# Optimization experiments

Hardware: AMD Instinct MI355X
Metric: run time of the kernel (lower is better)

Reference implementation:

```python
import jax, jax.numpy as jnp
import numpy as np

DIM = 768
D_STATE = 16
D_INNER = 2 * DIM  # expand=2


def setup_inputs() -> dict:
    key = jax.random.key(0)
    k_x, k_in, k_conv, k_out = jax.random.split(key, 4)
    B, L = 1, 4096
    x = jax.random.normal(k_x, (B, L, DIM), dtype=jnp.float32)
    # torch Linear weight layout: [out_features, in_features]
    W_in = jax.random.normal(k_in, (3 * D_INNER + 2 * D_STATE, DIM), dtype=jnp.float32) * 0.02
    # depthwise conv1d kernel: [out_ch=d_inner, in_ch/groups=1, k=3]
    W_conv = jax.random.normal(k_conv, (D_INNER, 1, 3), dtype=jnp.float32) * 0.1
    W_out = jax.random.normal(k_out, (DIM, D_INNER), dtype=jnp.float32) * 0.02
    A_log = jnp.log(jnp.tile(jnp.arange(1, D_STATE + 1, dtype=jnp.float32), (D_INNER, 1)))
    D = jnp.ones((D_INNER,), dtype=jnp.float32)
    return {"x": x, "W_in": W_in, "W_conv": W_conv, "W_out": W_out, "A_log": A_log, "D": D}


def reference(x, W_in, W_conv, W_out, A_log, D):
    d_inner = W_conv.shape[0]
    d_state = A_log.shape[1]
    Bsz = x.shape[0]

    xz = x @ W_in.T  # [B, L, 3*d_inner + 2*d_state]
    x_inner, z, B_ssm, C_ssm, delta = jnp.split(
        xz, [d_inner, 2 * d_inner, 2 * d_inner + d_state, 2 * d_inner + 2 * d_state], axis=-1
    )

    # depthwise conv over sequence: [B, d_inner, L]
    xc = jax.lax.conv_general_dilated(
        x_inner.transpose(0, 2, 1), W_conv,
        window_strides=(1,), padding=[(1, 1)], feature_group_count=d_inner,
    ).transpose(0, 2, 1)  # back to [B, L, d_inner]
    xc = jax.nn.silu(xc)

    A = -jnp.exp(A_log)  # [d_inner, d_state]
    delta = jax.nn.softplus(delta)  # [B, L, d_inner]
    dA = jnp.exp(jnp.einsum('bld,dn->bldn', delta, A))           # [B, L, d_inner, d_state]
    dBx = jnp.einsum('bld,bln,bld->bldn', delta, B_ssm, xc)      # delta_B * x fused

    def step(h, inp):
        da_t, dbx_t, c_t = inp  # [B,d,n], [B,d,n], [B,n]
        h = da_t * h + dbx_t
        y_t = jnp.einsum('bdn,bn->bd', h, c_t)
        return h, y_t

    h0 = jnp.zeros((Bsz, d_inner, d_state), dtype=x.dtype)
    _, ys = jax.lax.scan(
        step, h0,
        (dA.transpose(1, 0, 2, 3), dBx.transpose(1, 0, 2, 3), C_ssm.transpose(1, 0, 2)),
    )  # ys: [L, B, d_inner]

    y = ys.transpose(1, 0, 2) + xc * D  # skip connection
    y = y * jax.nn.silu(z)
    return y @ W_out.T  # [B, L, dim]
```

## Files before the change

### kernel.cpp

```cpp
#include <hip/hip_runtime.h>
#include <hip/hip_bf16.h>
#include <math.h>

#define LSEQ   4096
#define DIM    768
#define DINNER 1536
#define DSTATE 16
#define NCOLS  4640
#define NCH    128
#define CLEN   32
#define NPAD   4736
#define DXW    1568

typedef _Float16 f16;
typedef __attribute__((ext_vector_type(8))) _Float16 f16x8;
typedef __attribute__((ext_vector_type(4))) float f32x4;

__device__ __forceinline__ void gld_lds16(void* lds_dst, const void* gsrc) {
    __builtin_amdgcn_global_load_lds(
        (__attribute__((address_space(1))) void*)(gsrc),
        (__attribute__((address_space(3))) void*)(lds_dst), 16, 0, 0);
}

#define G1K    768
#define G1_NT  12
#define G1_BM  256
#define G1_BN  128
#define G1_RT  384
#define G1_LDSE (G1_RT * 64)

__global__ __launch_bounds__(512) void gemm1_pipe(const f16* __restrict__ A,
                                                  const f16* __restrict__ B,
                                                  float* __restrict__ C,
                                                  f16* __restrict__ Xb,
                                                  f16* __restrict__ Zb) {
    __shared__ __align__(16) f16 S[3 * G1_LDSE];

    const int P   = gridDim.x >> 3;
    const int idx = (blockIdx.x & 7) * P + (blockIdx.x >> 3);
    const int m0  = (idx & 15) * G1_BM;
    const int n0  = (idx >> 4) * G1_BN;

    const int tid  = threadIdx.x;
    const int w    = tid >> 6;
    const int lane = tid & 63;
    const int wr   = w >> 1;
    const int wc   = w & 1;
    const int m    = lane & 15;
    const int q    = lane >> 4;
    const int rl8  = lane >> 3;
    const int bsel = lane & 7;

    const f16* gb[6];
#pragma unroll
    for (int s = 0; s < 6; ++s) {
        const int rl  = (w + 8 * s) * 8 + rl8;
        const int blk = bsel ^ (rl & 7);
        gb[s] = (rl < G1_BM) ? A + (size_t)(m0 + rl) * G1K + blk * 8
                             : B + (size_t)(n0 + rl - G1_BM) * G1K + blk * 8;
    }

    f32x4 acc[4][4];
#pragma unroll
    for (int i = 0; i < 4; i++)
#pragma unroll
        for (int j = 0; j < 4; j++) acc[i][j] = (f32x4){0.f, 0.f, 0.f, 0.f};

    auto stg = [&](int kt) {
        f16* dst = S + (kt % 3) * G1_LDSE;
#pragma unroll
        for (int s = 0; s < 6; ++s)
            gld_lds16(dst + (w + 8 * s) * 512, gb[s] + kt * 64);
    };

    stg(0);
    stg(1);

#pragma unroll
    for (int kt = 0; kt < G1_NT; ++kt) {
        if (kt < G1_NT - 1) asm volatile("s_waitcnt vmcnt(6)" ::: "memory");
        else                asm volatile("s_waitcnt vmcnt(0)" ::: "memory");
        __builtin_amdgcn_s_barrier();
        if (kt + 2 < G1_NT) stg(kt + 2);

        const f16* As = S + (kt % 3) * G1_LDSE;
        const f16* Bs = As + G1_BM * 64;
        __builtin_amdgcn_s_setprio(1);
#pragma unroll
        for (int kk = 0; kk < 2; kk++) {
            const int fo = (((q + 4 * kk) ^ (m & 7)) << 3);
            f16x8 af[4], bh[4];
#pragma unroll
            for (int i = 0; i < 4; i++)
                af[i] = *(const f16x8*)&As[(wr * 64 + i * 16 + m) * 64 + fo];
#pragma unroll
            for (int j = 0; j < 4; j++)
                bh[j] = *(const f16x8*)&Bs[(wc * 64 + j * 16 + m) * 64 + fo];
#pragma unroll
            for (int i = 0; i < 4; i++)
#pragma unroll
                for (int j = 0; j < 4; j++)
                    acc[i][j] = __builtin_amdgcn_mfma_f32_16x16x32_f16(
                        af[i], bh[j], acc[i][j], 0, 0, 0);
        }
        __builtin_amdgcn_s_setprio(0);
    }

    if (n0 < DINNER) {
#pragma unroll
        for (int i = 0; i < 4; i++)
#pragma unroll
            for (int j = 0; j < 4; j++) {
                const int col  = n0 + wc * 64 + j * 16 + m;
                const int rowb = m0 + wr * 64 + i * 16 + q * 4;
#pragma unroll
                for (int r = 0; r < 4; r++)
                    Xb[(size_t)(rowb + r) * DINNER + col] = (f16)acc[i][j][r];
            }
        return;
    }
    if (n0 < 2 * DINNER) {
#pragma unroll
        for (int i = 0; i < 4; i++)
#pragma unroll
            for (int j = 0; j < 4; j++) {
                const int col  = n0 - DINNER + wc * 64 + j * 16 + m;
                const int rowb = m0 + wr * 64 + i * 16 + q * 4;
#pragma unroll
                for (int r = 0; r < 4; r++)
                    Zb[(size_t)(rowb + r) * DINNER + col] = (f16)acc[i][j][r];
            }
        return;
    }
#pragma unroll
    for (int i = 0; i < 4; i++)
#pragma unroll
        for (int j = 0; j < 4; j++) {
            const int col = n0 - 2 * DINNER + wc * 64 + j * 16 + m;
            if (col >= DXW) continue;
            const int rowb = m0 + wr * 64 + i * 16 + q * 4;
#pragma unroll
            for (int r = 0; r < 4; r++)
                C[(size_t)(rowb + r) * DXW + col] = acc[i][j][r];
        }
}

template<int BM, int BN, int WM, int WN, int NTB, bool COLM, bool ZMODE>
__global__ __launch_bounds__(256) void gemm_f16(const f16* __restrict__ A,
                                                const f16* __restrict__ B,
                                                float* __restrict__ C,
                                                f16* __restrict__ Xb,
                                                f16* __restrict__ Zb,
                                                int M, int N, int K, int ldc) {
    constexpr int MI  = WM / 16;
    constexpr int NI  = WN / 16;
    constexpr int NWN = BN / WN;
    constexpr int RT  = BM + BN;
    constexpr int NS  = RT / 8;

    __shared__ __align__(16) f16 S[RT * 64];
    f16* As = S;
    f16* Bs = S + BM * 64;

    const int P   = gridDim.x >> 3;
    const int idx = (blockIdx.x & 7) * P + (blockIdx.x >> 3);
    const int m0  = (COLM ? (idx % NTB) : (idx / NTB)) * BM;
    const int n0  = (COLM ? (idx / NTB) : (idx % NTB)) * BN;

    const int tid  = threadIdx.x;
    const int w    = tid >> 6;
    const int lane = tid & 63;
    const int wr   = w / NWN;
    const int wc   = w % NWN;
    const int m    = lane & 15;
    const int q    = lane >> 4;
    const int rl8  = lane >> 3;
    const int bsel = lane & 7;

    f32x4 acc[MI][NI];
#pragma unroll
    for (int i = 0; i < MI; i++)
#pragma unroll
        for (int j = 0; j < NI; j++) acc[i][j] = (f32x4){0.f, 0.f, 0.f, 0.f};

    for (int k0 = 0; k0 < K; k0 += 64) {
#pragma unroll
        for (int t = w; t < NS; t += 4) {
            const int rl  = t * 8 + rl8;
            const int blk = bsel ^ (rl & 7);
            const f16* g = (rl < BM)
                ? A + (size_t)(m0 + rl) * K + k0 + blk * 8
                : B + (size_t)(n0 + rl - BM) * K + k0 + blk * 8;
            gld_lds16(S + t * 8 * 64, g);
        }
        __syncthreads();

#pragma unroll
        for (int kk = 0; kk < 2; kk++) {
            const int fo = (((q + 4 * kk) ^ (m & 7)) << 3);
            f16x8 af[MI], bh[NI];
#pragma unroll
            for (int i = 0; i < MI; i++)
                af[i] = *(const f16x8*)&As[(wr * WM + i * 16 + m) * 64 + fo];
#pragma unroll
            for (int j = 0; j < NI; j++)
                bh[j] = *(const f16x8*)&Bs[(wc * WN + j * 16 + m) * 64 + fo];
#pragma unroll
            for (int i = 0; i < MI; i++)
#pragma unroll
                for (int j = 0; j < NI; j++)
                    acc[i][j] = __builtin_amdgcn_mfma_f32_16x16x32_f16(
                        af[i], bh[j], acc[i][j], 0, 0, 0);
        }
        __syncthreads();
    }

    if (ZMODE && n0 < DINNER) {
#pragma unroll
        for (int i = 0; i < MI; i++)
#pragma unroll
            for (int j = 0; j < NI; j++) {
                const int col  = n0 + wc * WN + j * 16 + m;
                const int rowb = m0 + wr * WM + i * 16 + q * 4;
#pragma unroll
                for (int r = 0; r < 4; r++)
                    Xb[(size_t)(rowb + r) * DINNER + col] = (f16)acc[i][j][r];
            }
        return;
    }
    if (ZMODE && n0 < 2 * DINNER) {
#pragma unroll
        for (int i = 0; i < MI; i++)
#pragma unroll
            for (int j = 0; j < NI; j++) {
                const int col  = n0 - DINNER + wc * WN + j * 16 + m;
                const int rowb = m0 + wr * WM + i * 16 + q * 4;
#pragma unroll
                for (int r = 0; r < 4; r++)
                    Zb[(size_t)(rowb + r) * DINNER + col] = (f16)acc[i][j][r];
            }
        return;
    }
#pragma unroll
    for (int i = 0; i < MI; i++)
#pragma unroll
        for (int j = 0; j < NI; j++) {
            const int col  = (ZMODE ? n0 - 2 * DINNER : n0) + wc * WN + j * 16 + m;
            const int lim  = ZMODE ? DXW : N;
            if (col >= lim) continue;
            const int rowb = m0 + wr * WM + i * 16 + q * 4;
#pragma unroll
            for (int r = 0; r < 4; r++)
                C[(size_t)(rowb + r) * ldc + col] = acc[i][j][r];
        }
}

#define E0 (LSEQ * DIM)
#define E1 (E0 + NPAD * DIM)
#define E2 (E1 + DIM * DINNER)

__global__ __launch_bounds__(256) void cvt_all(const float* __restrict__ x,
                                               const float* __restrict__ Wi,
                                               const float* __restrict__ Wo,
                                               f16* __restrict__ Ax,
                                               f16* __restrict__ Bw,
                                               f16* __restrict__ Bo) {
    int i = (blockIdx.x * 256 + threadIdx.x) * 4;
    if (i < E0) {
        float4 v = *(const float4*)(x + i);
        Ax[i] = (f16)v.x; Ax[i+1] = (f16)v.y; Ax[i+2] = (f16)v.z; Ax[i+3] = (f16)v.w;
    } else if (i < E1) {
        int e = i - E0;
        int n = e / DIM;
        if (n < NCOLS) {
            float4 v = *(const float4*)(Wi + e);
            Bw[e] = (f16)v.x; Bw[e+1] = (f16)v.y; Bw[e+2] = (f16)v.z; Bw[e+3] = (f16)v.w;
        } else {
            Bw[e] = (f16)0.f; Bw[e+1] = (f16)0.f; Bw[e+2] = (f16)0.f; Bw[e+3] = (f16)0.f;
        }
    } else if (i < E2) {
        int e = i - E1;
        float4 v = *(const float4*)(Wo + e);
        Bo[e] = (f16)v.x; Bo[e+1] = (f16)v.y; Bo[e+2] = (f16)v.z; Bo[e+3] = (f16)v.w;
    }
}

__global__ __launch_bounds__(256) void scan1_kernel(const float* __restrict__ Dxz,
                                                    const f16* __restrict__ Xb,
                                                    const float* __restrict__ Wc,
                                                    const float* __restrict__ A_log,
                                                    float* __restrict__ aprod,
                                                    float* __restrict__ hend) {
    __shared__ float Bs[CLEN * DSTATE];
    const int d  = blockIdx.x * 256 + threadIdx.x;
    const int c  = blockIdx.y;
    const int l0 = c * CLEN;
    for (int i = threadIdx.x; i < CLEN * DSTATE; i += 256)
        Bs[i] = Dxz[(size_t)(l0 + (i >> 4)) * DXW + (i & 15)];
    float Areg[DSTATE];
#pragma unroll
    for (int n = 0; n < DSTATE; n++) Areg[n] = -__expf(A_log[d * DSTATE + n]);
    const float w0 = Wc[d * 3 + 0], w1 = Wc[d * 3 + 1], w2 = Wc[d * 3 + 2];
    float xm = (l0 > 0) ? (float)Xb[(size_t)(l0 - 1) * DINNER + d] : 0.f;
    float x0 = (float)Xb[(size_t)l0 * DINNER + d];
    float ld_xp   = (float)Xb[(size_t)(l0 + 1) * DINNER + d];
    float ld_draw = Dxz[(size_t)l0 * DXW + 32 + d];
    __syncthreads();

    float h[DSTATE];
#pragma unroll
    for (int n = 0; n < DSTATE; n++) h[n] = 0.f;
    float S = 0.f;

    for (int t = 0; t < CLEN; t++) {
        const int l = l0 + t;
        float xp = ld_xp, draw = ld_draw;
        if (t + 1 < CLEN) {
            ld_xp   = (l + 2 < LSEQ) ? (float)Xb[(size_t)(l + 2) * DINNER + d] : 0.f;
            ld_draw = Dxz[(size_t)(l + 1) * DXW + 32 + d];
        }
        float v  = xm * w0 + x0 * w1 + xp * w2;
        float xcv = __fdividef(v, 1.f + __expf(-v));
        float dtv = (draw > 20.f) ? draw : __logf(1.f + __expf(draw));
        float u = dtv * xcv;
        S += dtv;
#pragma unroll
        for (int n = 0; n < DSTATE; n++) {
            float e = __expf(dtv * Areg[n]);
            h[n] = e * h[n] + u * Bs[t * DSTATE + n];
        }
        xm = x0; x0 = xp;
    }
#pragma unroll
    for (int n = 0; n < DSTATE; n++) {
        size_t idx = ((size_t)c * DSTATE + n) * DINNER + d;
        aprod[idx] = __expf(S * Areg[n]);
        hend[idx]  = h[n];
    }
}

__global__ __launch_bounds__(256) void scan2_kernel(const float* __restrict__ aprod,
                                                    const float* __restrict__ hend,
                                                    float* __restrict__ hinit) {
    const int g = blockIdx.x * 256 + threadIdx.x;
    const size_t S = (size_t)DSTATE * DINNER;
    size_t idx = g;
    float a = aprod[idx], e = hend[idx];
    float h = 0.f;
#pragma unroll 4
    for (int c = 0; c < NCH; c++) {
        float ac = a, ec = e;
        if (c + 1 < NCH) { a = aprod[idx + S]; e = hend[idx + S]; }
        hinit[idx] = h;
        h = ac * h + ec;
        idx += S;
    }
}

__global__ __launch_bounds__(256) void scan3_kernel(const float* __restrict__ Dxz,
                                                    const f16* __restrict__ Xb,
                                                    const f16* __restrict__ Zb,
                                                    const float* __restrict__ Wc,
                                                    const float* __restrict__ A_log,
                                                    const float* __restrict__ hinit,
                                                    const float* __restrict__ Dp,
                                                    f16* __restrict__ Ay) {
    __shared__ float Bs[CLEN * DSTATE];
    __shared__ float Cs[CLEN * DSTATE];
    const int d  = blockIdx.x * 256 + threadIdx.x;
    const int c  = blockIdx.y;
    const int l0 = c * CLEN;
    for (int i = threadIdx.x; i < CLEN * DSTATE; i += 256) {
        size_t roff = (size_t)(l0 + (i >> 4)) * DXW;
        Bs[i] = Dxz[roff + (i & 15)];
        Cs[i] = Dxz[roff + 16 + (i & 15)];
    }
    float Areg[DSTATE];
#pragma unroll
    for (int n = 0; n < DSTATE; n++) Areg[n] = -__expf(A_log[d * DSTATE + n]);
    float h[DSTATE];
#pragma unroll
    for (int n = 0; n < DSTATE; n++)
        h[n] = hinit[((size_t)c * DSTATE + n) * DINNER + d];
    const float Dv = Dp[d];
    const float w0 = Wc[d * 3 + 0], w1 = Wc[d * 3 + 1], w2 = Wc[d * 3 + 2];
    float xm = (l0 > 0) ? (float)Xb[(size_t)(l0 - 1) * DINNER + d] : 0.f;
    float x0 = (float)Xb[(size_t)l0 * DINNER + d];
    float ld_xp   = (float)Xb[(size_t)(l0 + 1) * DINNER + d];
    float ld_draw = Dxz[(size_t)l0 * DXW + 32 + d];
    float ld_z    = (float)Zb[(size_t)l0 * DINNER + d];
    __syncthreads();

    for (int t = 0; t < CLEN; t++) {
        const int l = l0 + t;
        float xp = ld_xp, draw = ld_draw, zv = ld_z;
        if (t + 1 < CLEN) {
            ld_xp   = (l + 2 < LSEQ) ? (float)Xb[(size_t)(l + 2) * DINNER + d] : 0.f;
            ld_draw = Dxz[(size_t)(l + 1) * DXW + 32 + d];
            ld_z    = (float)Zb[(size_t)(l + 1) * DINNER + d];
        }
        float v  = xm * w0 + x0 * w1 + xp * w2;
        float xcv = __fdividef(v, 1.f + __expf(-v));
        float dtv = (draw > 20.f) ? draw : __logf(1.f + __expf(draw));
        float u = dtv * xcv;
        float y = 0.f;
#pragma unroll
        for (int n = 0; n < DSTATE; n++) {
            float e = __expf(dtv * Areg[n]);
            h[n] = e * h[n] + u * Bs[t * DSTATE + n];
            y += h[n] * Cs[t * DSTATE + n];
        }
        float sz = __fdividef(zv, 1.f + __expf(-zv));
        Ay[(size_t)l * DINNER + d] = (f16)((y + xcv * Dv) * sz);
        xm = x0; x0 = xp;
    }
}

extern "C" void kernel_launch(void* const* d_in, const int* in_sizes, int n_in,
                              void* d_out, int out_size, void* d_ws, size_t ws_size,
                              hipStream_t stream) {
    const float* x     = (const float*)d_in[0];
    const float* W_in  = (const float*)d_in[1];
    const float* W_conv= (const float*)d_in[2];
    const float* W_out = (const float*)d_in[3];
    const float* A_log = (const float*)d_in[4];
    const float* Dp    = (const float*)d_in[5];
    float* out = (float*)d_out;

    float* ws  = (float*)d_ws;
    float* Dxz = ws;
    float* ap  = Dxz + (size_t)LSEQ * DXW;
    float* he  = ap + (size_t)NCH * DSTATE * DINNER;
    float* hi  = he + (size_t)NCH * DSTATE * DINNER;
    f16* Ax = (f16*)(hi + (size_t)NCH * DSTATE * DINNER);
    f16* Ay = Ax + (size_t)LSEQ * DIM;
    f16* Bw = Ay + (size_t)LSEQ * DINNER;
    f16* Bo = Bw + (size_t)NPAD * DIM;
    f16* Zb = Bo + (size_t)DIM * DINNER;
    f16* Xb = Zb + (size_t)LSEQ * DINNER;

    cvt_all<<<E2 / 1024, 256, 0, stream>>>(x, W_in, W_out, Ax, Bw, Bo);

    gemm1_pipe<<<592, 512, 0, stream>>>(Ax, Bw, Dxz, Xb, Zb);

    scan1_kernel<<<dim3(DINNER / 256, NCH), 256, 0, stream>>>(
        Dxz, Xb, W_conv, A_log, ap, he);
    scan2_kernel<<<(DINNER * DSTATE) / 256, 256, 0, stream>>>(ap, he, hi);
    scan3_kernel<<<dim3(DINNER / 256, NCH), 256, 0, stream>>>(
        Dxz, Xb, Zb, W_conv, A_log, hi, Dp, Ay);

    gemm_f16<64, 64, 32, 32, 12, false, false><<<768, 256, 0, stream>>>(
        Ay, Bo, out, nullptr, nullptr, LSEQ, DIM, DINNER, DIM);
}
```

Before: 245.1 us.

## Interleave GEMM prefetch with quadrant-split MFMA phases in in-projection kernel

```diff
diff --git a/kernel.cpp b/kernel.cpp
--- a/kernel.cpp
+++ b/kernel.cpp
@@ -66,43 +66,110 @@
 #pragma unroll
         for (int j = 0; j < 4; j++) acc[i][j] = (f32x4){0.f, 0.f, 0.f, 0.f};
 
-    auto stg = [&](int kt) {
+    auto stg2 = [&](int kt, int s0) {
+        f16* dst = S + (kt % 3) * G1_LDSE;
+#pragma unroll
+        for (int s = s0; s < s0 + 2; ++s)
+            gld_lds16(dst + (w + 8 * s) * 512, gb[s] + kt * 64);
+    };
+    auto stg6 = [&](int kt) {
         f16* dst = S + (kt % 3) * G1_LDSE;
 #pragma unroll
         for (int s = 0; s < 6; ++s)
             gld_lds16(dst + (w + 8 * s) * 512, gb[s] + kt * 64);
     };
 
-    stg(0);
-    stg(1);
+    stg6(0);
+    stg6(1);
 
 #pragma unroll
     for (int kt = 0; kt < G1_NT; ++kt) {
         if (kt < G1_NT - 1) asm volatile("s_waitcnt vmcnt(6)" ::: "memory");
         else                asm volatile("s_waitcnt vmcnt(0)" ::: "memory");
         __builtin_amdgcn_s_barrier();
-        if (kt + 2 < G1_NT) stg(kt + 2);
-
         const f16* As = S + (kt % 3) * G1_LDSE;
         const f16* Bs = As + G1_BM * 64;
+        const bool pf = (kt + 2 < G1_NT);
+
+        f16x8 af0[2][2], af2[2][2], bh0[2][2], bh2[2][2];
+
+#pragma unroll
+        for (int kk = 0; kk < 2; ++kk) {
+            const int fo = (((q + 4 * kk) ^ (m & 7)) << 3);
+#pragma unroll
+            for (int i = 0; i < 2; ++i) {
+                af0[kk][i] = *(const f16x8*)&As[(wr * 64 + i * 16 + m) * 64 + fo];
+                bh0[kk][i] = *(const f16x8*)&Bs[(wc * 64 + i * 16 + m) * 64 + fo];
+            }
+        }
+        if (pf) stg2(kt + 2, 0);
+        __builtin_amdgcn_s_barrier();
+        asm volatile("s_waitcnt lgkmcnt(0)" ::: "memory");
+        __builtin_amdgcn_sched_barrier(0);
         __builtin_amdgcn_s_setprio(1);
 #pragma unroll
-        for (int kk = 0; kk < 2; kk++) {
+        for (int kk = 0; kk < 2; ++kk)
+#pragma unroll
+            for (int i = 0; i < 2; ++i)
+#pragma unroll
+                for (int j = 0; j < 2; ++j)
+                    acc[i][j] = __builtin_amdgcn_mfma_f32_16x16x32_f16(
+                        af0[kk][i], bh0[kk][j], acc[i][j], 0, 0, 0);
+        __builtin_amdgcn_s_setprio(0);
+
+#pragma unroll
+        for (int kk = 0; kk < 2; ++kk) {
             const int fo = (((q + 4 * kk) ^ (m & 7)) << 3);
-            f16x8 af[4], bh[4];
-#pragma unroll
-            for (int i = 0; i < 4; i++)
-                af[i] = *(const f16x8*)&As[(wr * 64 + i * 16 + m) * 64 + fo];
-#pragma unroll
-            for (int j = 0; j < 4; j++)
-                bh[j] = *(const f16x8*)&Bs[(wc * 64 + j * 16 + m) * 64 + fo];
-#pragma unroll
-            for (int i = 0; i < 4; i++)
-#pragma unroll
-                for (int j = 0; j < 4; j++)
-                    acc[i][j] = __builtin_amdgcn_mfma_f32_16x16x32_f16(
-                        af[i], bh[j], acc[i][j], 0, 0, 0);
-        }
+#pragma unroll
+            for (int j = 0; j < 2; ++j)
+                bh2[kk][j] = *(const f16x8*)&Bs[(wc * 64 + (j + 2) * 16 + m) * 64 + fo];
+        }
+        if (pf) stg2(kt + 2, 2);
+        __builtin_amdgcn_s_barrier();
+        asm volatile("s_waitcnt lgkmcnt(0)" ::: "memory");
+        __builtin_amdgcn_sched_barrier(0);
+        __builtin_amdgcn_s_setprio(1);
+#pragma unroll
+        for (int kk = 0; kk < 2; ++kk)
+#pragma unroll
+            for (int i = 0; i < 2; ++i)
+#pragma unroll
+                for (int j = 0; j < 2; ++j)
+                    acc[i][j + 2] = __builtin_amdgcn_mfma_f32_16x16x32_f16(
+                        af0[kk][i], bh2[kk][j], acc[i][j + 2], 0, 0, 0);
+        __builtin_amdgcn_s_setprio(0);
+
+#pragma unroll
+        for (int kk = 0; kk < 2; ++kk) {
+            const int fo = (((q + 4 * kk) ^ (m & 7)) << 3);
+#pragma unroll
+            for (int i = 0; i < 2; ++i)
+                af2[kk][i] = *(const f16x8*)&As[(wr * 64 + (i + 2) * 16 + m) * 64 + fo];
+        }
+        if (pf) stg2(kt + 2, 4);
+        __builtin_amdgcn_s_barrier();
+        asm volatile("s_waitcnt lgkmcnt(0)" ::: "memory");
+        __builtin_amdgcn_sched_barrier(0);
+        __builtin_amdgcn_s_setprio(1);
+#pragma unroll
+        for (int kk = 0; kk < 2; ++kk)
+#pragma unroll
+            for (int i = 0; i < 2; ++i)
+#pragma unroll
+                for (int j = 0; j < 2; ++j)
+                    acc[i + 2][j] = __builtin_amdgcn_mfma_f32_16x16x32_f16(
+                        af2[kk][i], bh0[kk][j], acc[i + 2][j], 0, 0, 0);
+        __builtin_amdgcn_s_setprio(0);
+
+        __builtin_amdgcn_s_setprio(1);
+#pragma unroll
+        for (int kk = 0; kk < 2; ++kk)
+#pragma unroll
+            for (int i = 0; i < 2; ++i)
+#pragma unroll
+                for (int j = 0; j < 2; ++j)
+                    acc[i + 2][j + 2] = __builtin_amdgcn_mfma_f32_16x16x32_f16(
+                        af2[kk][i], bh2[kk][j], acc[i + 2][j + 2], 0, 0, 0);
         __builtin_amdgcn_s_setprio(0);
     }
 
```

Result: faster. 240.0 us (-2.1%).
